# Kernel tuning notes

Measured on AMD Instinct MI355X. Metric: run time of the kernel, lower is better.

Reference implementation:

```python
import jax, jax.numpy as jnp
import numpy as np

B, T, H, N_HEADS, HEAD_D = 16, 512, 1024, 16, 64
N_SKILLS, N_ITEMS = 50, 1000
VOCAB = 4 + 2 * N_ITEMS  # 2004
LN_EPS = 1e-3            # keras LayerNormalization default
PAD_NEG = -float(2 ** 32)


def position_encoding(length, hidden):
    # official transformer get_position_encoding: [sin | cos], then interleaved
    half = hidden // 2
    pos = jnp.arange(length, dtype=jnp.float32)[:, None]
    log_inc = np.log(1e4) / (half - 1)
    inv_ts = jnp.exp(jnp.arange(half, dtype=jnp.float32) * -log_inc)
    ang = pos * inv_ts[None, :]  # [T, H/2]
    pe = jnp.zeros((length, hidden), dtype=jnp.float32)
    pe = pe.at[:, 0::2].set(jnp.sin(ang))
    pe = pe.at[:, 1::2].set(jnp.cos(ang))
    return pe


def setup_inputs() -> dict:
    key = jax.random.key(0)
    ks = jax.random.split(key, 12)
    rng = np.random.default_rng(0)
    # binary Q-matrix [skills, items]; ensure every item has >=1 skill
    Qb = (rng.random((N_SKILLS, N_ITEMS)) < 0.1).astype(np.float32)
    Qb[rng.integers(0, N_SKILLS, size=N_ITEMS), np.arange(N_ITEMS)] = 1.0
    s = 0.02
    return {
        'prob_x': jax.random.randint(ks[0], (B, T), 4, VOCAB, dtype=jnp.int32),
        'prob_y2': jax.random.randint(ks[1], (B, T), 4, VOCAB, dtype=jnp.int32),
        'emb': jax.random.normal(ks[2], (VOCAB, H), jnp.float32) * s,
        'wq': jax.random.normal(ks[3], (H, N_HEADS, HEAD_D), jnp.float32) * s,
        'wk': jax.random.normal(ks[4], (H, N_HEADS, HEAD_D), jnp.float32) * s,
        'wv': jax.random.normal(ks[5], (H, N_HEADS, HEAD_D), jnp.float32) * s,
        'wo': jax.random.normal(ks[6], (N_HEADS, HEAD_D, H), jnp.float32) * s,
        'ln_gamma': jnp.ones((H,), jnp.float32),
        'ln_beta': jnp.zeros((H,), jnp.float32),
        'w_hid': jax.random.normal(ks[7], (H, 2 * N_SKILLS), jnp.float32) * s,
        'b_hid': jnp.zeros((2 * N_SKILLS,), jnp.float32),
        'w_skill': jax.random.normal(ks[8], (2 * N_SKILLS, N_SKILLS), jnp.float32) * s,
        'b_skill': jnp.zeros((N_SKILLS,), jnp.float32),
        'w_prob': jax.random.normal(ks[9], (N_SKILLS, N_ITEMS), jnp.float32) * s,
        'b_prob': jnp.zeros((N_ITEMS,), jnp.float32),
        'q_matrix': jnp.asarray(Qb),
    }


def reference(prob_x, prob_y2, emb, wq, wk, wv, wo, ln_gamma, ln_beta,
              w_hid, b_hid, w_skill, b_skill, w_prob, b_prob, q_matrix):
    Bq, Tq = prob_x.shape
    pid = (prob_x - 4) // 2        # item ids [B,T]
    next_pid = (prob_y2 - 4) // 2  # [B,T]

    x = emb[prob_x] + position_encoding(Tq, emb.shape[1])  # [B,T,H]

    # QKV projections (DenseEinsum, no bias)
    q = jnp.einsum('bth,hnd->btnd', x, wq) * (HEAD_D ** -0.5)
    k = jnp.einsum('bth,hnd->btnd', x, wk)
    v = jnp.einsum('bth,hnd->btnd', x, wv)

    logits = jnp.einsum('btnd,bfnd->bnft', k, q)  # [B,N,F,T]

    # causal future mask: 0 on/below diag, -inf above (1 - exp(1/tri - 1))
    causal = jnp.where(jnp.tril(jnp.ones((Tq, Tq), bool)), 0.0, -jnp.inf)
    logits = logits + causal[None, None]

    # item-item common-skill mask: -inf where items share no skill, 0 otherwise
    qtq = q_matrix.T @ q_matrix  # [I,I]
    items_items = jnp.where(qtq > 0, 0.0, -jnp.inf)
    sub = items_items[pid[:, 1:, None], pid[:, None, 1:]]  # [B,T-1,T-1]
    csm = jnp.pad(sub, ((0, 0), (1, 0), (1, 0)), constant_values=PAD_NEG)
    logits = logits + csm[:, None]  # broadcast over heads

    weights = jax.nn.softmax(logits, axis=-1)  # [B,N,F,T]
    attn = jnp.einsum('bnft,btnd->bfnd', weights, v)
    attn = jnp.einsum('bfnd,ndh->bfh', attn, wo)

    # add & layer-norm (keras default eps=1e-3)
    y = x + attn
    mu = jnp.mean(y, axis=-1, keepdims=True)
    var = jnp.var(y, axis=-1, keepdims=True)
    y = (y - mu) * jax.lax.rsqrt(var + LN_EPS) * ln_gamma + ln_beta

    h = jax.nn.relu(y @ w_hid + b_hid)
    skills = h @ w_skill + b_skill
    problems = jax.nn.sigmoid(skills @ w_prob + b_prob)  # [B,T,I]
    # einsum('abi,abi->ab', problems, one_hot(next_pid)) == gather
    out = jnp.take_along_axis(problems, next_pid[..., None], axis=-1)[..., 0]
    return out
```

## Files before the change

kernel.cpp:

```cpp
#include <hip/hip_runtime.h>
#include <hip/hip_bf16.h>

#define Bb 16
#define Tt 512
#define Hh 1024
#define NHd 16
#define HD 64
#define BT (Bb*Tt)
#define NSK 50
#define NIT 1000

typedef __attribute__((ext_vector_type(8))) short bf16x8;
typedef __attribute__((ext_vector_type(4))) float f32x4;
typedef unsigned short u16;
typedef unsigned int u32;
typedef unsigned long long u64;

__device__ inline u16 f2bf(float x){
  union { float f; u32 u; } v; v.f = x;
  u32 r = v.u + 0x7fffu + ((v.u >> 16) & 1u);
  return (u16)(r >> 16);
}
__device__ inline float bf2f(u32 u){
  union { u32 uu; float f; } v; v.uu = u << 16; return v.f;
}
__device__ inline void gload_lds16(const void* g, void* l){
  __builtin_amdgcn_global_load_lds(
    (const __attribute__((address_space(1))) u32*)g,
    (__attribute__((address_space(3))) u32*)l, 16, 0, 0);
}

__global__ __launch_bounds__(256) void k_prep(
    const int* __restrict__ prob_x, const float* __restrict__ qm,
    const float* __restrict__ wp,
    float* __restrict__ pe, u64* __restrict__ pmask, float* __restrict__ wpt)
{
  int z = blockIdx.z, bx = blockIdx.x, tid = threadIdx.x;
  if (z == 0){
    int h0 = tid*4, j0 = h0 >> 1;
    const float LOG_INC = 0.0180241495f;
    float a0 = (float)bx * expf(-(float)j0 * LOG_INC);
    float a1 = (float)bx * expf(-(float)(j0+1) * LOG_INC);
    float4 v = { sinf(a0), cosf(a0), sinf(a1), cosf(a1) };
    *(float4*)(pe + (size_t)bx*Hh + h0) = v;
  } else if (z == 1){
    if (bx >= BT/256) return;
    int i = bx*256 + tid;
    int pid = (prob_x[i] - 4) >> 1;
    u64 m = 0ull;
    #pragma unroll
    for (int s = 0; s < NSK; s++)
      if (qm[s*NIT + pid] != 0.f) m |= (1ull << s);
    pmask[i] = m;
  } else {
    int p = bx*4 + (tid >> 6), lane = tid & 63;
    if (p < NIT && lane < NSK) wpt[(size_t)p*64 + lane] = wp[(size_t)lane*NIT + p];
  }
}

__global__ __launch_bounds__(256) void k_wT_all(
    const float* __restrict__ wq, const float* __restrict__ wk,
    const float* __restrict__ wv, const float* __restrict__ wo,
    const float* __restrict__ wh, const float* __restrict__ gamma,
    const float* __restrict__ beta,
    u16* __restrict__ wqkvT, u16* __restrict__ woT, u16* __restrict__ whT,
    float2* __restrict__ uvp){
  int z = blockIdx.z;
  const float* src; u16* dst; int C = 1024; float scale = 1.f; bool useg = false;
  if      (z == 0){ src = wq; dst = wqkvT;                       scale = 0.125f; }
  else if (z == 1){ src = wk; dst = wqkvT + (size_t)1024*1024; }
  else if (z == 2){ src = wv; dst = wqkvT + (size_t)2*1024*1024; }
  else if (z == 3){ src = wo; dst = woT; }
  else            { src = wh; dst = whT; C = 100; useg = true; if (blockIdx.x >= 4) return; }

  __shared__ float tile[32][33];
  int tx = threadIdx.x & 31, ty = threadIdx.x >> 5;
  int c0 = blockIdx.x*32, r0 = blockIdx.y*32;
  #pragma unroll
  for (int i = 0; i < 32; i += 8){
    int r = r0 + ty + i, cc = c0 + tx;
    tile[ty+i][tx] = (cc < C) ? src[(size_t)r*C + cc] : 0.f;
  }
  __syncthreads();
  float gmul = useg ? gamma[r0 + tx] : scale;
  #pragma unroll
  for (int i = 0; i < 32; i += 8){
    int cc = c0 + ty + i, rr = r0 + tx;
    dst[(size_t)cc*1024 + rr] = f2bf(tile[tx][ty+i] * gmul);
  }
  if (useg && threadIdx.x < 32){
    int j = threadIdx.x;
    float us = 0.f, vs = 0.f;
    #pragma unroll
    for (int k = 0; k < 32; k++){
      float wv2 = tile[k][j];
      us += gamma[r0 + k] * wv2;
      vs += beta[r0 + k] * wv2;
    }
    uvp[(size_t)blockIdx.y*128 + c0 + j] = make_float2(us, vs);
  }
}

__global__ __launch_bounds__(256) void k_build_x2(
    const int* __restrict__ prob_x, const float* __restrict__ emb,
    const float* __restrict__ pe, u16* __restrict__ xb){
  int bt = blockIdx.x, tid = threadIdx.x;
  int t = bt & (Tt-1);
  int ix = prob_x[bt];
  int h = tid*4;
  float4 e = *(const float4*)(emb + (size_t)ix*Hh + h);
  float4 p = *(const float4*)(pe + (size_t)t*Hh + h);
  alignas(8) u16 tmp[4] = { f2bf(e.x+p.x), f2bf(e.y+p.y), f2bf(e.z+p.z), f2bf(e.w+p.w) };
  *(uint2*)(xb + (size_t)bt*Hh + h) = *(const uint2*)tmp;
}

__global__ __launch_bounds__(256) void k_gemm_qkv(
    const u16* __restrict__ A, const u16* __restrict__ Bt,
    u16* __restrict__ qb, u16* __restrict__ kb, u16* __restrict__ vtb)
{
  __shared__ u16 sA[128*64];
  __shared__ u16 sB[128*64];
  const int tid = threadIdx.x, w = tid >> 6, lane = tid & 63;
  const int c = lane & 15, g = lane >> 4;
  int lin = blockIdx.y*24 + blockIdx.x;
  int id2 = (lin & 7)*192 + (lin >> 3);
  int bx = id2 % 24, by = id2 / 24;
  const int row0 = by*128, col0 = bx*128;
  const int wr = w >> 1, wc = w & 1;
  const int srl = lane >> 3, scb = lane & 7;

  f32x4 acc[4][4];
  #pragma unroll
  for (int mi = 0; mi < 4; mi++)
    #pragma unroll
    for (int ni = 0; ni < 4; ni++) acc[mi][ni] = (f32x4){0.f,0.f,0.f,0.f};

  for (int k0 = 0; k0 < 1024; k0 += 64){
    __syncthreads();
    #pragma unroll
    for (int i = 0; i < 4; i++){
      int arow = 32*w + 8*i + srl;
      int kblk = scb ^ (arow & 7);
      gload_lds16(A  + (size_t)(row0 + arow)*1024 + k0 + kblk*8,
                  (char*)sA + w*4096 + i*1024);
      gload_lds16(Bt + (size_t)(col0 + arow)*1024 + k0 + kblk*8,
                  (char*)sB + w*4096 + i*1024);
    }
    __syncthreads();

    #pragma unroll
    for (int kh = 0; kh < 2; kh++){
      bf16x8 af[4], bf[4];
      #pragma unroll
      for (int mi = 0; mi < 4; mi++){
        int r = 64*wr + 16*mi + c;
        af[mi] = *(const bf16x8*)((char*)sA + r*128 + (((4*kh + g) ^ (r & 7))*16));
      }
      #pragma unroll
      for (int ni = 0; ni < 4; ni++){
        int r = 64*wc + 16*ni + c;
        bf[ni] = *(const bf16x8*)((char*)sB + r*128 + (((4*kh + g) ^ (r & 7))*16));
      }
      #pragma unroll
      for (int mi = 0; mi < 4; mi++)
        #pragma unroll
        for (int ni = 0; ni < 4; ni++)
          acc[mi][ni] = __builtin_amdgcn_mfma_f32_16x16x32_bf16(af[mi], bf[ni], acc[mi][ni], 0, 0, 0);
    }
  }

  int seg = col0 >> 10;
  int colL0 = col0 & 1023;
  if (seg < 2){
    u16* C = seg ? kb : qb;
    #pragma unroll
    for (int mi = 0; mi < 4; mi++){
      int m0 = row0 + 64*wr + 16*mi + 4*g;
      int bb = m0 >> 9, t0 = m0 & (Tt-1);
      #pragma unroll
      for (int ni = 0; ni < 4; ni++){
        int col = colL0 + 64*wc + 16*ni + c;
        int hd_ = col >> 6, d_ = col & 63;
        u16* base = C + (((size_t)bb*NHd + hd_)*Tt + t0)*HD + d_;
        #pragma unroll
        for (int r = 0; r < 4; r++) base[(size_t)r*HD] = f2bf(acc[mi][ni][r]);
      }
    }
  } else {
    #pragma unroll
    for (int mi = 0; mi < 4; mi++){
      int m0 = row0 + 64*wr + 16*mi + 4*g;
      int bb = m0 >> 9, t0 = m0 & (Tt-1);
      #pragma unroll
      for (int ni = 0; ni < 4; ni++){
        int col = colL0 + 64*wc + 16*ni + c;
        int hd_ = col >> 6, d_ = col & 63;
        alignas(8) u16 tmp[4];
        #pragma unroll
        for (int r = 0; r < 4; r++) tmp[r] = f2bf(acc[mi][ni][r]);
        *(uint2*)(vtb + (((size_t)bb*NHd + hd_)*HD + d_)*Tt + t0) = *(const uint2*)tmp;
      }
    }
  }
}

__global__ __launch_bounds__(256) void k_gemm_wo(
    const u16* __restrict__ A, const u16* __restrict__ Bt,
    u16* __restrict__ C, const u16* __restrict__ res, float2* __restrict__ stats)
{
  __shared__ u16 sA[128*64];
  __shared__ u16 sB[128*64];
  const int tid = threadIdx.x, w = tid >> 6, lane = tid & 63;
  const int c = lane & 15, g = lane >> 4;
  int lin = blockIdx.y*8 + blockIdx.x;
  int id2 = (lin & 7)*64 + (lin >> 3);
  int bx = id2 & 7, by = id2 >> 3;
  const int row0 = by*128, col0 = bx*128;
  const int wr = w >> 1, wc = w & 1;
  const int srl = lane >> 3, scb = lane & 7;

  f32x4 acc[4][4];
  #pragma unroll
  for (int mi = 0; mi < 4; mi++)
    #pragma unroll
    for (int ni = 0; ni < 4; ni++) acc[mi][ni] = (f32x4){0.f,0.f,0.f,0.f};

  for (int k0 = 0; k0 < 1024; k0 += 64){
    __syncthreads();
    #pragma unroll
    for (int i = 0; i < 4; i++){
      int arow = 32*w + 8*i + srl;
      int kblk = scb ^ (arow & 7);
      gload_lds16(A  + (size_t)(row0 + arow)*1024 + k0 + kblk*8,
                  (char*)sA + w*4096 + i*1024);
      gload_lds16(Bt + (size_t)(col0 + arow)*1024 + k0 + kblk*8,
                  (char*)sB + w*4096 + i*1024);
    }
    __syncthreads();

    #pragma unroll
    for (int kh = 0; kh < 2; kh++){
      bf16x8 af[4], bf[4];
      #pragma unroll
      for (int mi = 0; mi < 4; mi++){
        int r = 64*wr + 16*mi + c;
        af[mi] = *(const bf16x8*)((char*)sA + r*128 + (((4*kh + g) ^ (r & 7))*16));
      }
      #pragma unroll
      for (int ni = 0; ni < 4; ni++){
        int r = 64*wc + 16*ni + c;
        bf[ni] = *(const bf16x8*)((char*)sB + r*128 + (((4*kh + g) ^ (r & 7))*16));
      }
      #pragma unroll
      for (int mi = 0; mi < 4; mi++)
        #pragma unroll
        for (int ni = 0; ni < 4; ni++)
          acc[mi][ni] = __builtin_amdgcn_mfma_f32_16x16x32_bf16(af[mi], bf[ni], acc[mi][ni], 0, 0, 0);
    }
  }

  __syncthreads();
  float s1[4][4], s2[4][4];
  #pragma unroll
  for (int mi = 0; mi < 4; mi++)
    #pragma unroll
    for (int r = 0; r < 4; r++){ s1[mi][r] = 0.f; s2[mi][r] = 0.f; }

  #pragma unroll
  for (int mi = 0; mi < 4; mi++){
    int m0 = row0 + 64*wr + 16*mi + 4*g;
    #pragma unroll
    for (int ni = 0; ni < 4; ni++){
      int col = col0 + 64*wc + 16*ni + c;
      #pragma unroll
      for (int r = 0; r < 4; r++){
        size_t idx = (size_t)(m0 + r)*Hh + col;
        float yv = acc[mi][ni][r] + bf2f((u32)res[idx]);
        C[idx] = f2bf(yv);
        s1[mi][r] += yv; s2[mi][r] += yv*yv;
      }
    }
  }
  #pragma unroll
  for (int mi = 0; mi < 4; mi++)
    #pragma unroll
    for (int r = 0; r < 4; r++){
      #pragma unroll
      for (int off = 1; off < 16; off <<= 1){
        s1[mi][r] += __shfl_xor(s1[mi][r], off);
        s2[mi][r] += __shfl_xor(s2[mi][r], off);
      }
    }
  float (*sStat)[2][2] = (float(*)[2][2])sA;
  if (c == 0){
    #pragma unroll
    for (int mi = 0; mi < 4; mi++)
      #pragma unroll
      for (int r = 0; r < 4; r++){
        int ml = 64*wr + 16*mi + 4*g + r;
        sStat[ml][wc][0] = s1[mi][r];
        sStat[ml][wc][1] = s2[mi][r];
      }
  }
  __syncthreads();
  if (tid < 128){
    float a = sStat[tid][0][0] + sStat[tid][1][0];
    float b = sStat[tid][0][1] + sStat[tid][1][1];
    stats[(size_t)(row0 + tid)*8 + bx] = make_float2(a, b);
  }
}

__global__ __launch_bounds__(256) void k_gemm_hidden(
    const u16* __restrict__ A, const u16* __restrict__ Bt,
    const float2* __restrict__ stats, const float2* __restrict__ uvp,
    const float* __restrict__ b_hid, u16* __restrict__ C)
{
  __shared__ u16 sA[32*64];
  __shared__ u16 sB[128*64];
  __shared__ float sMu[32][2];
  __shared__ float2 sUV[128];
  const int tid = threadIdx.x, w = tid >> 6, lane = tid & 63;
  const int c = lane & 15, g = lane >> 4;
  const int row0 = blockIdx.x*32;
  const int srl = lane >> 3, scb = lane & 7;

  if (tid < 32){
    float m = 0.f, q = 0.f;
    #pragma unroll
    for (int cb = 0; cb < 8; cb++){
      float2 s = stats[(size_t)(row0 + tid)*8 + cb];
      m += s.x; q += s.y;
    }
    float mu = m * (1.f/Hh);
    float var = q * (1.f/Hh) - mu*mu;
    sMu[tid][0] = mu;
    sMu[tid][1] = rsqrtf(var + 1e-3f);
  }
  if (tid < 128){
    float us = 0.f, vs = 0.f;
    #pragma unroll 8
    for (int cb = 0; cb < 32; cb++){
      float2 p = uvp[(size_t)cb*128 + tid];
      us += p.x; vs += p.y;
    }
    float2 r = make_float2(0.f, 0.f);
    if (tid < 100){ r.x = us; r.y = vs + b_hid[tid]; }
    sUV[tid] = r;
  }

  f32x4 acc[2][2];
  #pragma unroll
  for (int mi = 0; mi < 2; mi++)
    #pragma unroll
    for (int ni = 0; ni < 2; ni++) acc[mi][ni] = (f32x4){0.f,0.f,0.f,0.f};

  for (int k0 = 0; k0 < 1024; k0 += 64){
    __syncthreads();
    {
      int arow = 8*w + srl;
      int kblk = scb ^ (arow & 7);
      gload_lds16(A + (size_t)(row0 + arow)*1024 + k0 + kblk*8,
                  (char*)sA + w*1024);
      #pragma unroll
      for (int i = 0; i < 4; i++){
        int brow = 32*w + 8*i + srl;
        int kb2 = scb ^ (brow & 7);
        gload_lds16(Bt + (size_t)brow*1024 + k0 + kb2*8,
                    (char*)sB + w*4096 + i*1024);
      }
    }
    __syncthreads();

    #pragma unroll
    for (int kh = 0; kh < 2; kh++){
      bf16x8 af[2], bf[2];
      #pragma unroll
      for (int mi = 0; mi < 2; mi++){
        int r = 16*mi + c;
        af[mi] = *(const bf16x8*)((char*)sA + r*128 + (((4*kh + g) ^ (r & 7))*16));
      }
      #pragma unroll
      for (int ni = 0; ni < 2; ni++){
        int r = 32*w + 16*ni + c;
        bf[ni] = *(const bf16x8*)((char*)sB + r*128 + (((4*kh + g) ^ (r & 7))*16));
      }
      #pragma unroll
      for (int mi = 0; mi < 2; mi++)
        #pragma unroll
        for (int ni = 0; ni < 2; ni++)
          acc[mi][ni] = __builtin_amdgcn_mfma_f32_16x16x32_bf16(af[mi], bf[ni], acc[mi][ni], 0, 0, 0);
    }
  }

  #pragma unroll
  for (int mi = 0; mi < 2; mi++){
    #pragma unroll
    for (int ni = 0; ni < 2; ni++){
      int col = 32*w + 16*ni + c;
      float2 uvv = sUV[col];
      #pragma unroll
      for (int r = 0; r < 4; r++){
        int ml = 16*mi + 4*g + r;
        float mu = sMu[ml][0], inv = sMu[ml][1];
        float h = fmaxf(inv*(acc[mi][ni][r] - mu*uvv.x) + uvv.y, 0.f);
        C[(size_t)(row0 + ml)*128 + col] = f2bf(h);
      }
    }
  }
}

__global__ __launch_bounds__(256, 3) void k_flash(
    const u16* __restrict__ qb, const u16* __restrict__ kb,
    const u16* __restrict__ vtb, const u64* __restrict__ pmask,
    u16* __restrict__ o)
{
  __shared__ u16 sK[2][64*64];
  __shared__ u16 sV[2][64*64];
  __shared__ u16 sP[4][32*64];

  const int tid = threadIdx.x;
  const int w = tid >> 6, lane = tid & 63;
  const int c = lane & 15, g = lane >> 4;
  const int bn = blockIdx.x;
  const int Fblk = 3 - blockIdx.y;
  const int b = bn >> 4, n = bn & 15;
  const int f0w = Fblk*128 + w*32;

  bf16x8 qf[2][2];
  #pragma unroll
  for (int fb = 0; fb < 2; fb++){
    const u16* qrow = qb + ((size_t)bn*Tt + f0w + 16*fb + c)*HD + 8*g;
    qf[fb][0] = *(const bf16x8*)(qrow);
    qf[fb][1] = *(const bf16x8*)(qrow + 32);
  }

  const u64* pmb = pmask + b*Tt;
  u64 mf[2][4];
  #pragma unroll
  for (int fb = 0; fb < 2; fb++)
    #pragma unroll
    for (int r = 0; r < 4; r++) mf[fb][r] = pmb[f0w + 16*fb + 4*g + r];

  f32x4 O[2][4];
  #pragma unroll
  for (int fb = 0; fb < 2; fb++)
    #pragma unroll
    for (int dt = 0; dt < 4; dt++) O[fb][dt] = (f32x4){0.f,0.f,0.f,0.f};
  float m_run[2][4], l_run[2][4];
  #pragma unroll
  for (int fb = 0; fb < 2; fb++)
    #pragma unroll
    for (int r = 0; r < 4; r++){ m_run[fb][r] = -1e30f; l_run[fb][r] = 0.f; }

  const char* kbase = (const char*)(kb + (size_t)bn*Tt*HD);
  const char* vbase = (const char*)(vtb + (size_t)bn*HD*Tt);
  char* sPw = (char*)(sP[w]);

  const int srow0 = 16*w + (lane >> 3);
  const int scb = lane & 7;

  #define STAGE(buf, T0)                                                          \
    {                                                                             \
      _Pragma("unroll")                                                           \
      for (int i = 0; i < 2; i++){                                                \
        int row = srow0 + 8*i;                                                    \
        int cb = scb ^ (row & 7);                                                 \
        gload_lds16(kbase + (size_t)((T0) + row)*128 + cb*16,                     \
                    (char*)sK[buf] + w*2048 + i*1024);                            \
        gload_lds16(vbase + (size_t)row*1024 + (T0)*2 + cb*16,                    \
                    (char*)sV[buf] + w*2048 + i*1024);                            \
      }                                                                           \
    }

  const int nT = 2*Fblk + 2;
  STAGE(0, 0)
  __syncthreads();
  int cur = 0;

  for (int it = 0; it < nT; ++it){
    const int t0 = it * 64;
    if (it + 1 < nT) STAGE(cur^1, (it+1)*64)

    if (t0 <= f0w + 31){
      const char* sKc = (const char*)sK[cur];
      const char* sVc = (const char*)sV[cur];

      f32x4 S[2][4];
      __builtin_amdgcn_s_setprio(1);
      #pragma unroll
      for (int ts = 0; ts < 4; ts++){
        int tl = ts*16 + c;
        const char* kr = sKc + tl*128;
        int sw = (tl & 7) << 4;
        bf16x8 kf0 = *(const bf16x8*)(kr + ((g*16) ^ sw));
        bf16x8 kf1 = *(const bf16x8*)(kr + ((64 + g*16) ^ sw));
        #pragma unroll
        for (int fb = 0; fb < 2; fb++){
          f32x4 a = (f32x4){0.f,0.f,0.f,0.f};
          a = __builtin_amdgcn_mfma_f32_16x16x32_bf16(qf[fb][0], kf0, a, 0, 0, 0);
          a = __builtin_amdgcn_mfma_f32_16x16x32_bf16(qf[fb][1], kf1, a, 0, 0, 0);
          S[fb][ts] = a;
        }
      }
      __builtin_amdgcn_s_setprio(0);

      u64 pmt[4];
      #pragma unroll
      for (int ts = 0; ts < 4; ts++) pmt[ts] = pmb[t0 + ts*16 + c];

      #pragma unroll
      for (int fb = 0; fb < 2; fb++){
        float al[4];
        #pragma unroll
        for (int r = 0; r < 4; r++){
          int frr = f0w + 16*fb + 4*g + r;
          u64 mfr = mf[fb][r];
          #pragma unroll
          for (int ts = 0; ts < 4; ts++){
            int t = t0 + ts*16 + c;
            bool ok = (frr == 0) ? (t == 0)
                     : (t > 0 && t <= frr && ((pmt[ts] & mfr) != 0ull));
            if (!ok) S[fb][ts][r] = -1e30f;
          }
          float mx = fmaxf(fmaxf(S[fb][0][r], S[fb][1][r]), fmaxf(S[fb][2][r], S[fb][3][r]));
          mx = fmaxf(mx, __shfl_xor(mx, 1));
          mx = fmaxf(mx, __shfl_xor(mx, 2));
          mx = fmaxf(mx, __shfl_xor(mx, 4));
          mx = fmaxf(mx, __shfl_xor(mx, 8));
          float mnew = fmaxf(m_run[fb][r], mx);
          al[r] = __expf(m_run[fb][r] - mnew);
          m_run[fb][r] = mnew;
          l_run[fb][r] *= al[r];
        }
        #pragma unroll
        for (int dt = 0; dt < 4; dt++)
          #pragma unroll
          for (int r = 0; r < 4; r++) O[fb][dt][r] *= al[r];

        #pragma unroll
        for (int ts = 0; ts < 4; ts++){
          #pragma unroll
          for (int r = 0; r < 4; r++){
            float pv = __expf(S[fb][ts][r] - m_run[fb][r]);
            l_run[fb][r] += pv;
            int prow = 16*fb + 4*g + r;
            int pbyte = (prow*128 + (ts*16 + c)*2) ^ ((prow & 7) << 4);
            *(u16*)(sPw + pbyte) = f2bf(pv);
          }
        }
      }

      bf16x8 pa[2][2];
      #pragma unroll
      for (int fb = 0; fb < 2; fb++){
        const char* pr = sPw + (16*fb + c)*128;
        int swp = (c & 7) << 4;
        pa[fb][0] = *(const bf16x8*)(pr + ((g*16) ^ swp));
        pa[fb][1] = *(const bf16x8*)(pr + ((64 + g*16) ^ swp));
      }
      __builtin_amdgcn_s_setprio(1);
      #pragma unroll
      for (int dt = 0; dt < 4; dt++){
        const char* vr = sVc + (dt*16 + c)*128;
        int swv = (c & 7) << 4;
        bf16x8 vf0 = *(const bf16x8*)(vr + ((g*16) ^ swv));
        bf16x8 vf1 = *(const bf16x8*)(vr + ((64 + g*16) ^ swv));
        #pragma unroll
        for (int fb = 0; fb < 2; fb++){
          O[fb][dt] = __builtin_amdgcn_mfma_f32_16x16x32_bf16(pa[fb][0], vf0, O[fb][dt], 0, 0, 0);
          O[fb][dt] = __builtin_amdgcn_mfma_f32_16x16x32_bf16(pa[fb][1], vf1, O[fb][dt], 0, 0, 0);
        }
      }
      __builtin_amdgcn_s_setprio(0);
    }

    __syncthreads();
    cur ^= 1;
  }
  #undef STAGE

  #pragma unroll
  for (int fb = 0; fb < 2; fb++){
    float inv[4];
    #pragma unroll
    for (int r = 0; r < 4; r++){
      float l = l_run[fb][r];
      l += __shfl_xor(l, 1);
      l += __shfl_xor(l, 2);
      l += __shfl_xor(l, 4);
      l += __shfl_xor(l, 8);
      inv[r] = 1.f / l;
    }
    u16* ob = o + ((size_t)(b*Tt + f0w + 16*fb))*Hh + n*HD;
    #pragma unroll
    for (int dt = 0; dt < 4; dt++)
      #pragma unroll
      for (int r = 0; r < 4; r++)
        ob[(size_t)(4*g + r)*Hh + dt*16 + c] = f2bf(O[fb][dt][r] * inv[r]);
  }
}

__global__ __launch_bounds__(256) void k_tail(
    const u16* __restrict__ hidden, const int* __restrict__ prob_y2,
    const float* __restrict__ w_skill, const float* __restrict__ b_skill,
    const float* __restrict__ wpt, const float* __restrict__ b_prob,
    float* __restrict__ out)
{
  __shared__ float shid[4][104];
  int w = threadIdx.x >> 6, lane = threadIdx.x & 63;
  int row = blockIdx.x*4 + w;
  if (lane < 50){
    u32 hp = *(const u32*)(hidden + (size_t)row*128 + 2*lane);
    shid[w][2*lane]   = bf2f(hp & 0xffffu);
    shid[w][2*lane+1] = bf2f(hp >> 16);
  }
  __syncthreads();
  float s = 0.f;
  if (lane < 50){
    s = b_skill[lane];
    #pragma unroll 4
    for (int i = 0; i < 100; i++) s += shid[w][i] * w_skill[i*NSK + lane];
  }
  int np = (prob_y2[row] - 4) >> 1;
  float z = (lane < 50) ? s * wpt[(size_t)np*64 + lane] : 0.f;
  #pragma unroll
  for (int off = 1; off < 64; off <<= 1) z += __shfl_xor(z, off);
  if (lane == 0) out[row] = 1.f/(1.f + expf(-(z + b_prob[np])));
}

extern "C" void kernel_launch(void* const* d_in, const int* in_sizes, int n_in,
                              void* d_out, int out_size, void* d_ws, size_t ws_size,
                              hipStream_t stream)
{
  const int*   prob_x   = (const int*)d_in[0];
  const int*   prob_y2  = (const int*)d_in[1];
  const float* emb      = (const float*)d_in[2];
  const float* wq       = (const float*)d_in[3];
  const float* wk       = (const float*)d_in[4];
  const float* wv       = (const float*)d_in[5];
  const float* wo       = (const float*)d_in[6];
  const float* ln_g     = (const float*)d_in[7];
  const float* ln_b     = (const float*)d_in[8];
  const float* w_hid    = (const float*)d_in[9];
  const float* b_hid    = (const float*)d_in[10];
  const float* w_skill  = (const float*)d_in[11];
  const float* b_skill  = (const float*)d_in[12];
  const float* w_prob   = (const float*)d_in[13];
  const float* b_prob   = (const float*)d_in[14];
  const float* q_matrix = (const float*)d_in[15];
  float* out = (float*)d_out;

  char* ws = (char*)d_ws;
  const size_t M16 = (size_t)BT*Hh*2;
  u16*   xb     = (u16*)(ws);
  u16*   qb     = (u16*)(ws + M16);
  u16*   kb     = (u16*)(ws + 2*M16);
  u16*   vtb    = (u16*)(ws + 3*M16);
  u16*   att    = (u16*)(ws + 4*M16);
  u16*   y      = qb;
  u16*   hidden = kb;
  char*  aux    = ws + 5*M16;
  float* pe     = (float*)(aux);
  u16*   wqkvT  = (u16*)(aux + (size_t)2*1024*1024);
  u16*   woT    = wqkvT + (size_t)3*1024*1024;
  u16*   whT    = woT + (size_t)1024*1024;
  float* wpt    = (float*)(whT + (size_t)128*1024);
  u64*   pmask  = (u64*)(wpt + (size_t)NIT*64);
  float2* stats = (float2*)((char*)pmask + (size_t)BT*8);
  float2* uvp   = (float2*)((char*)stats + (size_t)BT*8*sizeof(float2));

  k_prep<<<dim3(512,1,3), 256, 0, stream>>>(prob_x, q_matrix, w_prob, pe, pmask, wpt);
  k_wT_all<<<dim3(32,32,5), 256, 0, stream>>>(wq, wk, wv, wo, w_hid, ln_g, ln_b,
                                              wqkvT, woT, whT, uvp);
  k_build_x2<<<BT, 256, 0, stream>>>(prob_x, emb, pe, xb);

  k_gemm_qkv<<<dim3(24,64), 256, 0, stream>>>(xb, wqkvT, qb, kb, vtb);

  k_flash<<<dim3(Bb*NHd, 4), 256, 0, stream>>>(qb, kb, vtb, pmask, att);

  k_gemm_wo<<<dim3(8,64), 256, 0, stream>>>(att, woT, y, xb, stats);

  k_gemm_hidden<<<256, 256, 0, stream>>>(y, whT, stats, uvp, b_hid, hidden);

  k_tail<<<BT/4, 256, 0, stream>>>(hidden, prob_y2, w_skill, b_skill, wpt, b_prob, out);
}
```

Measured before the change: 207.9 us.

## Fold prep kernel into weight transpose, inline position encoding, transpose flash S tiles

Removes the separate prep kernel. The mask and w_prob transpose work moves into extra z-slices of the weight-transpose launch, and the sinusoidal position encoding is computed inline with fast intrinsics during embedding build instead of being stored and reloaded. In the flash kernel the MFMA operand order is swapped so each lane owns one query row. That turns the row max and sum reductions into two cross-group shuffles, cuts mask registers, and allows packed 8-byte P and output stores. Fast __sinf/__cosf on large angles may lose accuracy.

```diff
diff --git a/kernel.cpp b/kernel.cpp
--- a/kernel.cpp
+++ b/kernel.cpp
@@ -24,38 +24,13 @@
 __device__ inline float bf2f(u32 u){
   union { u32 uu; float f; } v; v.uu = u << 16; return v.f;
 }
+__device__ inline u32 pack2bf(float lo, float hi){
+  return (u32)f2bf(lo) | ((u32)f2bf(hi) << 16);
+}
 __device__ inline void gload_lds16(const void* g, void* l){
   __builtin_amdgcn_global_load_lds(
     (const __attribute__((address_space(1))) u32*)g,
     (__attribute__((address_space(3))) u32*)l, 16, 0, 0);
-}
-
-__global__ __launch_bounds__(256) void k_prep(
-    const int* __restrict__ prob_x, const float* __restrict__ qm,
-    const float* __restrict__ wp,
-    float* __restrict__ pe, u64* __restrict__ pmask, float* __restrict__ wpt)
-{
-  int z = blockIdx.z, bx = blockIdx.x, tid = threadIdx.x;
-  if (z == 0){
-    int h0 = tid*4, j0 = h0 >> 1;
-    const float LOG_INC = 0.0180241495f;
-    float a0 = (float)bx * expf(-(float)j0 * LOG_INC);
-    float a1 = (float)bx * expf(-(float)(j0+1) * LOG_INC);
-    float4 v = { sinf(a0), cosf(a0), sinf(a1), cosf(a1) };
-    *(float4*)(pe + (size_t)bx*Hh + h0) = v;
-  } else if (z == 1){
-    if (bx >= BT/256) return;
-    int i = bx*256 + tid;
-    int pid = (prob_x[i] - 4) >> 1;
-    u64 m = 0ull;
-    #pragma unroll
-    for (int s = 0; s < NSK; s++)
-      if (qm[s*NIT + pid] != 0.f) m |= (1ull << s);
-    pmask[i] = m;
-  } else {
-    int p = bx*4 + (tid >> 6), lane = tid & 63;
-    if (p < NIT && lane < NSK) wpt[(size_t)p*64 + lane] = wp[(size_t)lane*NIT + p];
-  }
 }
 
 __global__ __launch_bounds__(256) void k_wT_all(
@@ -63,9 +38,30 @@
     const float* __restrict__ wv, const float* __restrict__ wo,
     const float* __restrict__ wh, const float* __restrict__ gamma,
     const float* __restrict__ beta,
+    const int* __restrict__ prob_x, const float* __restrict__ qm,
+    const float* __restrict__ wp,
     u16* __restrict__ wqkvT, u16* __restrict__ woT, u16* __restrict__ whT,
-    float2* __restrict__ uvp){
+    float2* __restrict__ uvp, u64* __restrict__ pmask, float* __restrict__ wpt){
   int z = blockIdx.z;
+  int tid = threadIdx.x;
+  if (z == 5){
+    if (blockIdx.y) return;
+    int i = blockIdx.x*256 + tid;
+    int pid = (prob_x[i] - 4) >> 1;
+    u64 m = 0ull;
+    #pragma unroll
+    for (int s = 0; s < NSK; s++)
+      if (qm[s*NIT + pid] != 0.f) m |= (1ull << s);
+    pmask[i] = m;
+    return;
+  }
+  if (z == 6){
+    int blk = blockIdx.y*32 + blockIdx.x;
+    if (blk >= 250) return;
+    int p = blk*4 + (tid >> 6), lane = tid & 63;
+    if (lane < NSK) wpt[(size_t)p*64 + lane] = wp[(size_t)lane*NIT + p];
+    return;
+  }
   const float* src; u16* dst; int C = 1024; float scale = 1.f; bool useg = false;
   if      (z == 0){ src = wq; dst = wqkvT;                       scale = 0.125f; }
   else if (z == 1){ src = wk; dst = wqkvT + (size_t)1024*1024; }
@@ -74,7 +70,7 @@
   else            { src = wh; dst = whT; C = 100; useg = true; if (blockIdx.x >= 4) return; }
 
   __shared__ float tile[32][33];
-  int tx = threadIdx.x & 31, ty = threadIdx.x >> 5;
+  int tx = tid & 31, ty = tid >> 5;
   int c0 = blockIdx.x*32, r0 = blockIdx.y*32;
   #pragma unroll
   for (int i = 0; i < 32; i += 8){
@@ -88,8 +84,8 @@
     int cc = c0 + ty + i, rr = r0 + tx;
     dst[(size_t)cc*1024 + rr] = f2bf(tile[tx][ty+i] * gmul);
   }
-  if (useg && threadIdx.x < 32){
-    int j = threadIdx.x;
+  if (useg && tid < 32){
+    int j = tid;
     float us = 0.f, vs = 0.f;
     #pragma unroll
     for (int k = 0; k < 32; k++){
@@ -103,14 +99,18 @@
 
 __global__ __launch_bounds__(256) void k_build_x2(
     const int* __restrict__ prob_x, const float* __restrict__ emb,
-    const float* __restrict__ pe, u16* __restrict__ xb){
+    u16* __restrict__ xb){
   int bt = blockIdx.x, tid = threadIdx.x;
   int t = bt & (Tt-1);
   int ix = prob_x[bt];
   int h = tid*4;
   float4 e = *(const float4*)(emb + (size_t)ix*Hh + h);
-  float4 p = *(const float4*)(pe + (size_t)t*Hh + h);
-  alignas(8) u16 tmp[4] = { f2bf(e.x+p.x), f2bf(e.y+p.y), f2bf(e.z+p.z), f2bf(e.w+p.w) };
+  const float LOG_INC = 0.0180241495f;
+  int j0 = h >> 1;
+  float a0 = (float)t * __expf(-(float)j0 * LOG_INC);
+  float a1 = (float)t * __expf(-(float)(j0+1) * LOG_INC);
+  alignas(8) u16 tmp[4] = { f2bf(e.x + __sinf(a0)), f2bf(e.y + __cosf(a0)),
+                            f2bf(e.z + __sinf(a1)), f2bf(e.w + __cosf(a1)) };
   *(uint2*)(xb + (size_t)bt*Hh + h) = *(const uint2*)tmp;
 }
 
@@ -435,22 +435,17 @@
   }
 
   const u64* pmb = pmask + b*Tt;
-  u64 mf[2][4];
+  int frow[2]; u64 mf[2];
+  #pragma unroll
+  for (int fb = 0; fb < 2; fb++){ frow[fb] = f0w + 16*fb + c; mf[fb] = pmb[frow[fb]]; }
+
+  f32x4 O[2][4];
   #pragma unroll
   for (int fb = 0; fb < 2; fb++)
     #pragma unroll
-    for (int r = 0; r < 4; r++) mf[fb][r] = pmb[f0w + 16*fb + 4*g + r];
-
-  f32x4 O[2][4];
-  #pragma unroll
-  for (int fb = 0; fb < 2; fb++)
-    #pragma unroll
     for (int dt = 0; dt < 4; dt++) O[fb][dt] = (f32x4){0.f,0.f,0.f,0.f};
-  float m_run[2][4], l_run[2][4];
-  #pragma unroll
-  for (int fb = 0; fb < 2; fb++)
-    #pragma unroll
-    for (int r = 0; r < 4; r++){ m_run[fb][r] = -1e30f; l_run[fb][r] = 0.f; }
+  float m_run[2] = {-1e30f, -1e30f};
+  float l_run[2] = {0.f, 0.f};
 
   const char* kbase = (const char*)(kb + (size_t)bn*Tt*HD);
   const char* vbase = (const char*)(vtb + (size_t)bn*HD*Tt);
@@ -497,78 +492,86 @@
         #pragma unroll
         for (int fb = 0; fb < 2; fb++){
           f32x4 a = (f32x4){0.f,0.f,0.f,0.f};
-          a = __builtin_amdgcn_mfma_f32_16x16x32_bf16(qf[fb][0], kf0, a, 0, 0, 0);
-          a = __builtin_amdgcn_mfma_f32_16x16x32_bf16(qf[fb][1], kf1, a, 0, 0, 0);
+          a = __builtin_amdgcn_mfma_f32_16x16x32_bf16(kf0, qf[fb][0], a, 0, 0, 0);
+          a = __builtin_amdgcn_mfma_f32_16x16x32_bf16(kf1, qf[fb][1], a, 0, 0, 0);
           S[fb][ts] = a;
         }
       }
       __builtin_amdgcn_s_setprio(0);
 
-      u64 pmt[4];
-      #pragma unroll
-      for (int ts = 0; ts < 4; ts++) pmt[ts] = pmb[t0 + ts*16 + c];
+      u64 pmt[4][4];
+      #pragma unroll
+      for (int ts = 0; ts < 4; ts++){
+        const u64* pp = pmb + t0 + 16*ts + 4*g;
+        pmt[ts][0] = pp[0]; pmt[ts][1] = pp[1];
+        pmt[ts][2] = pp[2]; pmt[ts][3] = pp[3];
+      }
 
       #pragma unroll
       for (int fb = 0; fb < 2; fb++){
-        float al[4];
-        #pragma unroll
-        for (int r = 0; r < 4; r++){
-          int frr = f0w + 16*fb + 4*g + r;
-          u64 mfr = mf[fb][r];
-          #pragma unroll
-          for (int ts = 0; ts < 4; ts++){
-            int t = t0 + ts*16 + c;
-            bool ok = (frr == 0) ? (t == 0)
-                     : (t > 0 && t <= frr && ((pmt[ts] & mfr) != 0ull));
-            if (!ok) S[fb][ts][r] = -1e30f;
-          }
-          float mx = fmaxf(fmaxf(S[fb][0][r], S[fb][1][r]), fmaxf(S[fb][2][r], S[fb][3][r]));
-          mx = fmaxf(mx, __shfl_xor(mx, 1));
-          mx = fmaxf(mx, __shfl_xor(mx, 2));
-          mx = fmaxf(mx, __shfl_xor(mx, 4));
-          mx = fmaxf(mx, __shfl_xor(mx, 8));
-          float mnew = fmaxf(m_run[fb][r], mx);
-          al[r] = __expf(m_run[fb][r] - mnew);
-          m_run[fb][r] = mnew;
-          l_run[fb][r] *= al[r];
-        }
-        #pragma unroll
-        for (int dt = 0; dt < 4; dt++)
-          #pragma unroll
-          for (int r = 0; r < 4; r++) O[fb][dt][r] *= al[r];
-
+        int f = frow[fb];
+        u64 mfr = mf[fb];
         #pragma unroll
         for (int ts = 0; ts < 4; ts++){
           #pragma unroll
           for (int r = 0; r < 4; r++){
-            float pv = __expf(S[fb][ts][r] - m_run[fb][r]);
-            l_run[fb][r] += pv;
-            int prow = 16*fb + 4*g + r;
-            int pbyte = (prow*128 + (ts*16 + c)*2) ^ ((prow & 7) << 4);
-            *(u16*)(sPw + pbyte) = f2bf(pv);
+            int t = t0 + 16*ts + 4*g + r;
+            bool ok = (f == 0) ? (t == 0)
+                     : (t > 0 && t <= f && ((pmt[ts][r] & mfr) != 0ull));
+            if (!ok) S[fb][ts][r] = -1e30f;
           }
         }
+        float mx = -1e30f;
+        #pragma unroll
+        for (int ts = 0; ts < 4; ts++)
+          #pragma unroll
+          for (int r = 0; r < 4; r++) mx = fmaxf(mx, S[fb][ts][r]);
+        mx = fmaxf(mx, __shfl_xor(mx, 16));
+        mx = fmaxf(mx, __shfl_xor(mx, 32));
+        float mnew = fmaxf(m_run[fb], mx);
+        float al = __expf(m_run[fb] - mnew);
+        m_run[fb] = mnew;
+        l_run[fb] *= al;
+        #pragma unroll
+        for (int dt = 0; dt < 4; dt++) O[fb][dt] *= al;
+
+        int prow = 16*fb + c;
+        int swz = (prow & 7) << 4;
+        float lsum = 0.f;
+        #pragma unroll
+        for (int ts = 0; ts < 4; ts++){
+          float p0 = __expf(S[fb][ts][0] - mnew);
+          float p1 = __expf(S[fb][ts][1] - mnew);
+          float p2 = __expf(S[fb][ts][2] - mnew);
+          float p3 = __expf(S[fb][ts][3] - mnew);
+          lsum += (p0 + p1) + (p2 + p3);
+          uint2 dw = { pack2bf(p0, p1), pack2bf(p2, p3) };
+          *(uint2*)(sPw + prow*128 + ((32*ts + 8*g) ^ swz)) = dw;
+        }
+        l_run[fb] += lsum;
       }
 
       bf16x8 pa[2][2];
       #pragma unroll
       for (int fb = 0; fb < 2; fb++){
-        const char* pr = sPw + (16*fb + c)*128;
-        int swp = (c & 7) << 4;
-        pa[fb][0] = *(const bf16x8*)(pr + ((g*16) ^ swp));
-        pa[fb][1] = *(const bf16x8*)(pr + ((64 + g*16) ^ swp));
+        int prow = 16*fb + c;
+        int swz = (prow & 7) << 4;
+        const char* pr = sPw + prow*128;
+        pa[fb][0] = *(const bf16x8*)(pr + ((16*g) ^ swz));
+        pa[fb][1] = *(const bf16x8*)(pr + ((64 + 16*g) ^ swz));
       }
       __builtin_amdgcn_s_setprio(1);
       #pragma unroll
       for (int dt = 0; dt < 4; dt++){
-        const char* vr = sVc + (dt*16 + c)*128;
-        int swv = (c & 7) << 4;
+        int vl = dt*16 + c;
+        const char* vr = sVc + vl*128;
+        int swv = (vl & 7) << 4;
         bf16x8 vf0 = *(const bf16x8*)(vr + ((g*16) ^ swv));
         bf16x8 vf1 = *(const bf16x8*)(vr + ((64 + g*16) ^ swv));
         #pragma unroll
         for (int fb = 0; fb < 2; fb++){
-          O[fb][dt] = __builtin_amdgcn_mfma_f32_16x16x32_bf16(pa[fb][0], vf0, O[fb][dt], 0, 0, 0);
-          O[fb][dt] = __builtin_amdgcn_mfma_f32_16x16x32_bf16(pa[fb][1], vf1, O[fb][dt], 0, 0, 0);
+          O[fb][dt] = __builtin_amdgcn_mfma_f32_16x16x32_bf16(vf0, pa[fb][0], O[fb][dt], 0, 0, 0);
+          O[fb][dt] = __builtin_amdgcn_mfma_f32_16x16x32_bf16(vf1, pa[fb][1], O[fb][dt], 0, 0, 0);
         }
       }
       __builtin_amdgcn_s_setprio(0);
@@ -581,22 +584,18 @@
 
   #pragma unroll
   for (int fb = 0; fb < 2; fb++){
-    float inv[4];
-    #pragma unroll
-    for (int r = 0; r < 4; r++){
-      float l = l_run[fb][r];
-      l += __shfl_xor(l, 1);
-      l += __shfl_xor(l, 2);
-      l += __shfl_xor(l, 4);
-      l += __shfl_xor(l, 8);
-      inv[r] = 1.f / l;
-    }
-    u16* ob = o + ((size_t)(b*Tt + f0w + 16*fb))*Hh + n*HD;
-    #pragma unroll
-    for (int dt = 0; dt < 4; dt++)
-      #pragma unroll
-      for (int r = 0; r < 4; r++)
-        ob[(size_t)(4*g + r)*Hh + dt*16 + c] = f2bf(O[fb][dt][r] * inv[r]);
+    float l = l_run[fb];
+    l += __shfl_xor(l, 16);
+    l += __shfl_xor(l, 32);
+    float inv = 1.f / l;
+    u16* ob = o + ((size_t)(b*Tt + frow[fb]))*Hh + n*HD;
+    #pragma unroll
+    for (int dt = 0; dt < 4; dt++){
+      alignas(8) u16 tmp[4];
+      #pragma unroll
+      for (int r = 0; r < 4; r++) tmp[r] = f2bf(O[fb][dt][r] * inv);
+      *(uint2*)(ob + dt*16 + 4*g) = *(const uint2*)tmp;
+    }
   }
 }
 
@@ -660,8 +659,7 @@
   u16*   y      = qb;
   u16*   hidden = kb;
   char*  aux    = ws + 5*M16;
-  float* pe     = (float*)(aux);
-  u16*   wqkvT  = (u16*)(aux + (size_t)2*1024*1024);
+  u16*   wqkvT  = (u16*)(aux);
   u16*   woT    = wqkvT + (size_t)3*1024*1024;
   u16*   whT    = woT + (size_t)1024*1024;
   float* wpt    = (float*)(whT + (size_t)128*1024);
@@ -669,10 +667,10 @@
   float2* stats = (float2*)((char*)pmask + (size_t)BT*8);
   float2* uvp   = (float2*)((char*)stats + (size_t)BT*8*sizeof(float2));
 
-  k_prep<<<dim3(512,1,3), 256, 0, stream>>>(prob_x, q_matrix, w_prob, pe, pmask, wpt);
-  k_wT_all<<<dim3(32,32,5), 256, 0, stream>>>(wq, wk, wv, wo, w_hid, ln_g, ln_b,
-                                              wqkvT, woT, whT, uvp);
-  k_build_x2<<<BT, 256, 0, stream>>>(prob_x, emb, pe, xb);
+  k_wT_all<<<dim3(32,32,7), 256, 0, stream>>>(wq, wk, wv, wo, w_hid, ln_g, ln_b,
+                                              prob_x, q_matrix, w_prob,
+                                              wqkvT, woT, whT, uvp, pmask, wpt);
+  k_build_x2<<<BT, 256, 0, stream>>>(prob_x, emb, xb);
 
   k_gemm_qkv<<<dim3(24,64), 256, 0, stream>>>(xb, wqkvT, qb, kb, vtb);
 
```

Result: faster. 180.7 us (-13.1%).
